# Kernel tuning notes

Measured on AMD Instinct MI355X. Metric: run time of the kernel, lower is better.

## Reference

```python
import jax, jax.numpy as jnp
import numpy as np

HID_DIM = 1024
B, S = 8, 2048
SCALE = float(np.sqrt(HID_DIM))
NEG = -1e10


def setup_inputs() -> dict:
    key = jax.random.key(0)
    ks = jax.random.split(key, 13)
    d = HID_DIM
    std = 1.0 / np.sqrt(d)
    return {
        "query": jax.random.normal(ks[0], (B, S, d), jnp.float32),
        "key_": jax.random.normal(ks[1], (B, S, d), jnp.float32),
        "value": jax.random.normal(ks[2], (B, S, d), jnp.float32),
        "mask": jax.random.randint(ks[3], (B, S), 0, 2, jnp.int32),
        "Wq": jax.random.uniform(ks[4], (d, d), jnp.float32, -std, std),
        "bq": jax.random.uniform(ks[5], (d,), jnp.float32, -std, std),
        "Wk": jax.random.uniform(ks[6], (d, d), jnp.float32, -std, std),
        "bk": jax.random.uniform(ks[7], (d,), jnp.float32, -std, std),
        "Wv": jax.random.uniform(ks[8], (d, d), jnp.float32, -std, std),
        "bv": jax.random.uniform(ks[9], (d,), jnp.float32, -std, std),
        "Wfc": jax.random.uniform(ks[10], (d, d), jnp.float32, -std, std),
        "bfc": jax.random.uniform(ks[11], (d,), jnp.float32, -std, std),
    }


def reference(query, key_, value, mask, Wq, bq, Wk, bk, Wv, bv, Wfc, bfc):
    # Linear projections (torch Linear: x @ W.T + b)
    Q = jnp.einsum("bsd,ed->bse", query, Wq) + bq
    K = jnp.einsum("bsd,ed->bse", key_, Wk) + bk
    V = jnp.einsum("bsd,ed->bse", value, Wv) + bv
    # Scaled dot-product energy: [B, S, S]
    energy = jnp.einsum("bqd,bkd->bqk", Q, K) / SCALE
    # Faithful to source: mask broadcast over last dim masks QUERY rows
    energy = jnp.where(mask[:, :, None] == 0, NEG, energy)
    attention = jax.nn.softmax(energy, axis=-1)  # dropout=0 (eval)
    x = jnp.einsum("bqk,bkd->bqd", attention, V)
    out = jnp.einsum("bsd,ed->bse", x, Wfc) + bfc
    return out
```

## Files before the change

kernel.cpp:

```cpp
#include <hip/hip_runtime.h>
#include <hip/hip_bf16.h>


#define DEVINL __device__ __forceinline__

typedef __bf16 bf16x8 __attribute__((ext_vector_type(8)));
typedef float f32x4 __attribute__((ext_vector_type(4)));

static constexpr int Bb = 8;
static constexpr int S = 2048;
static constexpr int D = 1024;

DEVINL unsigned short f32_to_bf16(float f) {
  unsigned u = __float_as_uint(f);
  u = (u + 0x7FFFu + ((u >> 16) & 1u)) >> 16;
  return (unsigned short)u;
}
DEVINL float bflo(unsigned u) { return __uint_as_float(u << 16); }
DEVINL float bfhi(unsigned u) { return __uint_as_float(u & 0xFFFF0000u); }

DEVINL void gload16(const unsigned short* g, char* l) {
  __builtin_amdgcn_global_load_lds((__attribute__((address_space(1))) void*)g,
                                   (__attribute__((address_space(3))) void*)l,
                                   16, 0, 0);
}
DEVINL void gload16u(const unsigned short* g, unsigned short* l) {
  gload16(g, (char*)l);
}

#define BAR() __builtin_amdgcn_s_barrier()
#define LGK0() asm volatile("s_waitcnt lgkmcnt(0)" ::: "memory")

#define PH_OPEN() \
  BAR();          \
  LGK0();         \
  __builtin_amdgcn_s_setprio(1)
#define PH_CLOSE()               \
  __builtin_amdgcn_s_setprio(0); \
  BAR()

#define MFMA_QUAD(A_, B_, MO, NO)                                              \
  {                                                                            \
    _Pragma("unroll") for (int mi_ = 0; mi_ < 4; mi_++) {                      \
      _Pragma("unroll") for (int nj_ = 0; nj_ < 2; nj_++) {                    \
        acc[(MO) + mi_][(NO) + nj_] = __builtin_amdgcn_mfma_f32_16x16x32_bf16( \
            A_[mi_][0], B_[nj_][0], acc[(MO) + mi_][(NO) + nj_], 0, 0, 0);     \
        acc[(MO) + mi_][(NO) + nj_] = __builtin_amdgcn_mfma_f32_16x16x32_bf16( \
            A_[mi_][1], B_[nj_][1], acc[(MO) + mi_][(NO) + nj_], 0, 0, 0);     \
      }                                                                        \
    }                                                                          \
  }

__global__ __launch_bounds__(256) void conv_f32_bf16(const float* __restrict__ in,
                                                     unsigned short* __restrict__ out,
                                                     int n8) {
  int i = blockIdx.x * 256 + threadIdx.x;
  int stride = gridDim.x * 256;
  for (; i < n8; i += stride) {
    const float4* p = (const float4*)in + (size_t)i * 2;
    float4 a = p[0], b = p[1];
    uint4 o;
    o.x = (unsigned)f32_to_bf16(a.x) | ((unsigned)f32_to_bf16(a.y) << 16);
    o.y = (unsigned)f32_to_bf16(a.z) | ((unsigned)f32_to_bf16(a.w) << 16);
    o.z = (unsigned)f32_to_bf16(b.x) | ((unsigned)f32_to_bf16(b.y) << 16);
    o.w = (unsigned)f32_to_bf16(b.z) | ((unsigned)f32_to_bf16(b.w) << 16);
    ((uint4*)out)[i] = o;
  }
}

__global__ __launch_bounds__(256) void tconv(const float* __restrict__ in,
                                             unsigned short* __restrict__ out,
                                             int R, int C) {
  __shared__ unsigned short t[64][72];
  const int c0 = blockIdx.x * 64, r0 = blockIdx.y * 64, b = blockIdx.z;
  in += (size_t)b * R * C;
  out += (size_t)b * R * C;
  const int tr = threadIdx.x >> 4;
  const int tc = threadIdx.x & 15;
#pragma unroll
  for (int i = 0; i < 4; i++) {
    int row = tr + i * 16;
    float4 v = *(const float4*)(in + (size_t)(r0 + row) * C + c0 + tc * 4);
    t[tc * 4 + 0][row] = f32_to_bf16(v.x);
    t[tc * 4 + 1][row] = f32_to_bf16(v.y);
    t[tc * 4 + 2][row] = f32_to_bf16(v.z);
    t[tc * 4 + 3][row] = f32_to_bf16(v.w);
  }
  __syncthreads();
  const int c = threadIdx.x >> 2, rs = (threadIdx.x & 3) * 16;
  unsigned short tmp[16];
#pragma unroll
  for (int j = 0; j < 16; j++) tmp[j] = t[c][rs + j];
  *(uint4*)(out + (size_t)(c0 + c) * R + r0 + rs) = *(const uint4*)&tmp[0];
  *(uint4*)(out + (size_t)(c0 + c) * R + r0 + rs + 8) = *(const uint4*)&tmp[8];
}

__global__ __launch_bounds__(256) void cvec_kernel(const float* __restrict__ Wfc,
                                                   const float* __restrict__ bv,
                                                   const float* __restrict__ bfc,
                                                   float* __restrict__ cv) {
  const int f = blockIdx.x;
  const float* row = Wfc + (size_t)f * 1024;
  float s = 0.f;
  for (int e = threadIdx.x; e < 1024; e += 256) s += row[e] * bv[e];
#pragma unroll
  for (int off = 32; off >= 1; off >>= 1) s += __shfl_xor(s, off);
  __shared__ float red[4];
  const int wave = threadIdx.x >> 6, lane = threadIdx.x & 63;
  if (lane == 0) red[wave] = s;
  __syncthreads();
  if (threadIdx.x == 0) cv[f] = red[0] + red[1] + red[2] + red[3] + bfc[f];
}

__global__ __launch_bounds__(256) void gvec_kernel(const unsigned short* __restrict__ WkT,
                                                   const float* __restrict__ bq,
                                                   float* __restrict__ g32) {
  const int e = blockIdx.x;
  const unsigned short* row = WkT + (size_t)e * 1024;
  const int j0 = threadIdx.x * 4;
  uint2 v = *(const uint2*)(row + j0);
  float4 b4 = *(const float4*)(bq + j0);
  float s = bflo(v.x) * b4.x + bfhi(v.x) * b4.y + bflo(v.y) * b4.z + bfhi(v.y) * b4.w;
#pragma unroll
  for (int off = 32; off >= 1; off >>= 1) s += __shfl_xor(s, off);
  __shared__ float red[4];
  const int wave = threadIdx.x >> 6, lane = threadIdx.x & 63;
  if (lane == 0) red[wave] = s;
  __syncthreads();
  if (threadIdx.x == 0) g32[e] = (red[0] + red[1] + red[2] + red[3]) * (1.0f / 32.0f);
}

__global__ __launch_bounds__(256) void wvec_kernel(const unsigned short* __restrict__ xk,
                                                   const float* __restrict__ g32,
                                                   float* __restrict__ w32) {
  const int row = blockIdx.x * 4 + (threadIdx.x >> 6);
  const int lane = threadIdx.x & 63;
  const unsigned short* r = xk + (size_t)row * 1024;
  float s = 0.f;
#pragma unroll
  for (int c = 0; c < 2; c++) {
    const int e0 = c * 512 + lane * 8;
    uint4 v = *(const uint4*)(r + e0);
    unsigned u[4] = {v.x, v.y, v.z, v.w};
#pragma unroll
    for (int i = 0; i < 4; i++) {
      float2 gg = *(const float2*)(g32 + e0 + i * 2);
      s += bflo(u[i]) * gg.x + bfhi(u[i]) * gg.y;
    }
  }
#pragma unroll
  for (int off = 32; off >= 1; off >>= 1) s += __shfl_xor(s, off);
  if (lane == 0) w32[row] = s;
}

__global__ __launch_bounds__(256) void mask_scan(const int* __restrict__ msk,
                                                 int* __restrict__ qidx,
                                                 int* __restrict__ midx,
                                                 int* __restrict__ cnts) {
  __shared__ int offs[257];
  const int b = blockIdx.x;
  const int* mrow = msk + b * 2048;
  const int base = threadIdx.x * 8;
  int m[8], c = 0;
#pragma unroll
  for (int i = 0; i < 8; i++) {
    m[i] = mrow[base + i];
    c += m[i];
  }
  offs[threadIdx.x + 1] = c;
  __syncthreads();
  if (threadIdx.x == 0) {
    offs[0] = 0;
    for (int j = 1; j <= 256; j++) offs[j] += offs[j - 1];
    int tot = offs[256];
    cnts[b] = tot;
    cnts[8 + b] = (tot + 127) & ~127;
    cnts[16 + b] = (tot + 255) & ~255;
    cnts[24 + b] = 2048 - tot;
  }
  __syncthreads();
  int u = offs[threadIdx.x];
#pragma unroll
  for (int i = 0; i < 8; i++) {
    int idx = base + i;
    if (m[i])
      qidx[b * 2048 + (u++)] = idx;
    else
      midx[b * 2048 + (idx - u)] = idx;
  }
}

__global__ __launch_bounds__(128) void compact_q(const float* __restrict__ q,
                                                 const int* __restrict__ qidx,
                                                 const int* __restrict__ cnts,
                                                 unsigned short* __restrict__ xqC) {
  const int r = blockIdx.x;
  const int b = r >> 11, i = r & 2047;
  if (i >= cnts[16 + b]) return;
  unsigned short* dst = xqC + ((size_t)b * 2048 + i) * 1024;
  if (i < cnts[b]) {
    const float* src = q + ((size_t)b * 2048 + qidx[b * 2048 + i]) * 1024 + threadIdx.x * 8;
    float4 a = *(const float4*)src;
    float4 c = *(const float4*)(src + 4);
    uint4 o;
    o.x = (unsigned)f32_to_bf16(a.x) | ((unsigned)f32_to_bf16(a.y) << 16);
    o.y = (unsigned)f32_to_bf16(a.z) | ((unsigned)f32_to_bf16(a.w) << 16);
    o.z = (unsigned)f32_to_bf16(c.x) | ((unsigned)f32_to_bf16(c.y) << 16);
    o.w = (unsigned)f32_to_bf16(c.z) | ((unsigned)f32_to_bf16(c.w) << 16);
    ((uint4*)dst)[threadIdx.x] = o;
  } else {
    ((uint4*)dst)[threadIdx.x] = make_uint4(0, 0, 0, 0);
  }
}

__global__ __launch_bounds__(64) void colmean_kernel(const unsigned short* __restrict__ vpT,
                                                     const float* __restrict__ cv,
                                                     float* __restrict__ cm) {
  const int f = blockIdx.x, b = blockIdx.y;
  const unsigned short* base = vpT + (size_t)f * 16384 + b * 2048 + threadIdx.x * 32;
  float s = 0.f;
#pragma unroll
  for (int c = 0; c < 4; c++) {
    uint4 v = ((const uint4*)base)[c];
    unsigned u[4] = {v.x, v.y, v.z, v.w};
#pragma unroll
    for (int i = 0; i < 4; i++) s += bflo(u[i]) + bfhi(u[i]);
  }
#pragma unroll
  for (int off = 32; off >= 1; off >>= 1) s += __shfl_xor(s, off);
  if (threadIdx.x == 0) cm[b * 1024 + f] = s * (1.0f / 2048.0f) + cv[f];
}

__global__ __launch_bounds__(128) void fill_masked(const int* __restrict__ midx,
                                                   const int* __restrict__ cnts,
                                                   const float* __restrict__ cm,
                                                   float* __restrict__ out) {
  const int r = blockIdx.x;
  const int b = r >> 11, j = r & 2047;
  if (j >= cnts[24 + b]) return;
  const int qr = midx[b * 2048 + j];
  float* dst = out + ((size_t)b * 2048 + qr) * 1024 + threadIdx.x * 8;
  const float* src = cm + b * 1024 + threadIdx.x * 8;
  *(float4*)dst = *(const float4*)src;
  *(float4*)(dst + 4) = *(const float4*)(src + 4);
}

__global__ __launch_bounds__(256) void rowinv_kernel(const float* __restrict__ partialT,
                                                     float* __restrict__ rowinv) {
  const int r = blockIdx.x * 256 + threadIdx.x;
  float s = 0.f;
#pragma unroll
  for (int c = 0; c < 32; c++) s += partialT[(size_t)c * 16384 + r];
  rowinv[r] = 1.0f / s;
}

__global__ __launch_bounds__(256) void gemm128(const unsigned short* __restrict__ A,
                                               const unsigned short* __restrict__ Bt,
                                               unsigned short* __restrict__ C,
                                               int M, int N, int K,
                                               long long bsA, long long bsB, long long bsC) {
  const int tid = threadIdx.x;
  const int wave = tid >> 6;
  const int lane = tid & 63;
  const int wr = wave >> 1, wc = wave & 1;
  const int m0 = blockIdx.y * 128, n0 = blockIdx.x * 128;
  A += (size_t)blockIdx.z * bsA;
  Bt += (size_t)blockIdx.z * bsB;
  C += (size_t)blockIdx.z * bsC;

  __shared__ unsigned short lds[2][2][128 * 32];

  const int srow = wave * 16 + (lane >> 2);
  const int scol = (lane & 3) * 8;
  const unsigned short* gA = A + (size_t)(m0 + srow) * K + scol;
  const unsigned short* gB = Bt + (size_t)(n0 + srow) * K + scol;

  f32x4 acc[4][4];
#pragma unroll
  for (int i = 0; i < 4; i++)
#pragma unroll
    for (int j = 0; j < 4; j++) acc[i][j] = (f32x4){0.f, 0.f, 0.f, 0.f};

  const int nk = K >> 5;
  auto stage = [&](int buf, int kt) {
    const unsigned short* a0 = gA + (size_t)kt * 32;
    const unsigned short* b0 = gB + (size_t)kt * 32;
    unsigned short* la = &lds[buf][0][wave * 512];
    unsigned short* lb = &lds[buf][1][wave * 512];
    gload16u(a0, la);
    gload16u(a0 + (size_t)64 * K, la + 2048);
    gload16u(b0, lb);
    gload16u(b0 + (size_t)64 * K, lb + 2048);
  };

  stage(0, 0);
  asm volatile("s_waitcnt vmcnt(0)" ::: "memory");
  __syncthreads();

  const int fm = lane & 15;
  const int fk = (lane >> 4) * 8;

  int cur = 0;
  for (int t = 0; t < nk; ++t) {
    if (t + 1 < nk) stage(cur ^ 1, t + 1);
    bf16x8 af[4], bfr[4];
#pragma unroll
    for (int i = 0; i < 4; i++)
      af[i] = *(const bf16x8*)&lds[cur][0][(wr * 64 + i * 16 + fm) * 32 + fk];
#pragma unroll
    for (int j = 0; j < 4; j++)
      bfr[j] = *(const bf16x8*)&lds[cur][1][(wc * 64 + j * 16 + fm) * 32 + fk];
#pragma unroll
    for (int i = 0; i < 4; i++)
#pragma unroll
      for (int j = 0; j < 4; j++)
        acc[i][j] = __builtin_amdgcn_mfma_f32_16x16x32_bf16(af[i], bfr[j], acc[i][j], 0, 0, 0);
    asm volatile("s_waitcnt vmcnt(0)" ::: "memory");
    __syncthreads();
    cur ^= 1;
  }

  const int en = n0 + wc * 64 + fm;
  const int em = m0 + wr * 64 + ((lane >> 4) << 2);
#pragma unroll
  for (int j = 0; j < 4; j++)
#pragma unroll
    for (int i = 0; i < 4; i++)
#pragma unroll
      for (int r = 0; r < 4; r++)
        C[(size_t)(em + i * 16 + r) * N + en + j * 16] = f32_to_bf16(acc[i][j][r]);
}

__global__ __launch_bounds__(512, 1) void gemmE(
    const unsigned short* __restrict__ A, const unsigned short* __restrict__ Bt,
    const float* __restrict__ w32, const int* __restrict__ cnts,
    float* __restrict__ partialT, unsigned short* __restrict__ E, float scale) {
  extern __shared__ char smem[];
  const int tid = threadIdx.x;
  const int wave = tid >> 6, lane = tid & 63;
  const int wrM = wave >> 1, wcN = wave & 1;

  const int nwg = 16 * 8 * 8;
  const int wg = blockIdx.x + 16 * (blockIdx.y + 8 * blockIdx.z);
  const int swz = (wg & 7) * (nwg >> 3) + (wg >> 3);
  const int bx = swz % 16;
  const int rem = swz / 16;
  const int by = rem % 8;
  const int bz = rem / 8;

  const int n0 = bx * 128;
  if (n0 >= cnts[8 + bz]) return;
  const int m0 = by * 256;
  A += (size_t)bz * 2048 * 1024;
  Bt += (size_t)bz * 2048 * 1024;

  const int rl = lane >> 3;
  const int gl = (lane & 7) ^ rl;
  const unsigned short* gA = A + (size_t)(m0 + wave * 8 + rl) * 1024 + gl * 8;
  const unsigned short* gB = Bt + (size_t)(n0 + wave * 8 + rl) * 1024 + gl * 8;

  auto stage = [&](int db, int t) {
    char* base = smem + db * 49152;
    const unsigned short* ga = gA + (size_t)t * 64;
    const unsigned short* gb = gB + (size_t)t * 64;
#pragma unroll
    for (int c = 0; c < 4; c++)
      gload16(ga + (size_t)c * 64 * 1024, base + c * 8192 + wave * 1024);
#pragma unroll
    for (int c = 0; c < 2; c++)
      gload16(gb + (size_t)c * 64 * 1024, base + 32768 + c * 8192 + wave * 1024);
  };

  const int fr = lane & 15;
  const int fg = lane >> 4;
  auto readA = [&](int db, int mi, int kc) -> bf16x8 {
    const int row = wrM * 64 + mi * 16 + fr;
    const int g = (kc * 4 + fg) ^ (row & 7);
    return *(const bf16x8*)(smem + db * 49152 + row * 128 + g * 16);
  };
  auto readB = [&](int db, int nj, int kc) -> bf16x8 {
    const int row = wcN * 64 + nj * 16 + fr;
    const int g = (kc * 4 + fg) ^ (row & 7);
    return *(const bf16x8*)(smem + db * 49152 + 32768 + row * 128 + g * 16);
  };

  f32x4 acc[4][4];
#pragma unroll
  for (int i = 0; i < 4; i++)
#pragma unroll
    for (int j = 0; j < 4; j++) acc[i][j] = (f32x4){0.f, 0.f, 0.f, 0.f};

  const int nt = 16;
  stage(0, 0);
  stage(1, 1);
  asm volatile("s_waitcnt vmcnt(6)" ::: "memory");
  BAR();

  for (int t = 0; t < nt; ++t) {
    const int db = t % 3;
    bf16x8 a[4][2], b0[2][2], b1[2][2];
#pragma unroll
    for (int mi = 0; mi < 4; mi++) { a[mi][0] = readA(db, mi, 0); a[mi][1] = readA(db, mi, 1); }
#pragma unroll
    for (int nj = 0; nj < 2; nj++) { b0[nj][0] = readB(db, nj, 0); b0[nj][1] = readB(db, nj, 1); }
    BAR();
    LGK0();
    if (t + 2 < nt) stage((t + 2) % 3, t + 2);
    __builtin_amdgcn_s_setprio(1);
    MFMA_QUAD(a, b0, 0, 0);
    __builtin_amdgcn_s_setprio(0);
    BAR();
#pragma unroll
    for (int nj = 0; nj < 2; nj++) { b1[nj][0] = readB(db, nj + 2, 0); b1[nj][1] = readB(db, nj + 2, 1); }
    BAR();
    LGK0();
    __builtin_amdgcn_s_setprio(1);
    MFMA_QUAD(a, b1, 0, 2);
    __builtin_amdgcn_s_setprio(0);
    if (t + 2 < nt)
      asm volatile("s_waitcnt vmcnt(6)" ::: "memory");
    else
      asm volatile("s_waitcnt vmcnt(0)" ::: "memory");
    BAR();
  }

  const int keyrow0 = m0 + wrM * 64 + fg * 4;
  const int colq = wcN * 64 + fr;
  float psum[4] = {0.f, 0.f, 0.f, 0.f};
#pragma unroll
  for (int mi = 0; mi < 4; mi++) {
    const int krow = keyrow0 + mi * 16;
    const float4 w4 = *(const float4*)&w32[bz * 2048 + krow];
    const int lrow = wrM * 64 + fg * 4 + mi * 16;
#pragma unroll
    for (int nj = 0; nj < 4; nj++) {
      float p0 = __expf(fmaf(acc[mi][nj][0], scale, w4.x));
      float p1 = __expf(fmaf(acc[mi][nj][1], scale, w4.y));
      float p2 = __expf(fmaf(acc[mi][nj][2], scale, w4.z));
      float p3 = __expf(fmaf(acc[mi][nj][3], scale, w4.w));
      psum[nj] += (p0 + p1) + (p2 + p3);
      unsigned lo = (unsigned)f32_to_bf16(p0) | ((unsigned)f32_to_bf16(p1) << 16);
      unsigned hi = (unsigned)f32_to_bf16(p2) | ((unsigned)f32_to_bf16(p3) << 16);
      const int c = colq + nj * 16;
      const int byte = c * 512 + ((((lrow >> 3) ^ (c & 7)) << 4) | ((lrow & 4) << 1));
      *(uint2*)(smem + byte) = make_uint2(lo, hi);
    }
  }
#pragma unroll
  for (int nj = 0; nj < 4; nj++) {
    psum[nj] += __shfl_xor(psum[nj], 16);
    psum[nj] += __shfl_xor(psum[nj], 32);
  }
  if (fg == 0) {
#pragma unroll
    for (int nj = 0; nj < 4; nj++)
      partialT[(size_t)(by * 4 + wrM) * 16384 + bz * 2048 + n0 + colq + nj * 16] = psum[nj];
  }
  __syncthreads();
  unsigned short* Eb = E + (size_t)bz * S * S;
  const int qh = wave * 2 + (lane >> 5);
  const int kl = (lane & 31) * 8;
#pragma unroll
  for (int p = 0; p < 8; p++) {
    const int ql = qh + p * 16;
    const int byte = ql * 512 + ((((kl >> 3) ^ (ql & 7)) << 4));
    uint4 vv = *(const uint4*)(smem + byte);
    *(uint4*)(Eb + (size_t)(n0 + ql) * 2048 + m0 + kl) = vv;
  }
}

template <int OUTMODE, bool HAS_BIAS, int EXITMODE>
__global__ __launch_bounds__(512, 2) void gemm256(
    const unsigned short* __restrict__ A, const unsigned short* __restrict__ Bt,
    const float* __restrict__ bias, const int* __restrict__ cnts,
    const int* __restrict__ qidx, float* __restrict__ partial,
    void* __restrict__ Cv, int M, int N, int K, int lda, int ldb,
    long long bsA, long long bsB, long long bsC, float scale) {
  extern __shared__ char smem[];
  const int tid = threadIdx.x;
  const int wave = tid >> 6, lane = tid & 63;
  const int wr = wave >> 2, wc = wave & 3;

  const int gx = gridDim.x, gy = gridDim.y;
  const int nwg = gx * gy * (int)gridDim.z;
  const int wg = blockIdx.x + gx * (blockIdx.y + gy * blockIdx.z);
  const int swz = (wg & 7) * (nwg >> 3) + (wg >> 3);
  const int bx = swz % gx;
  const int rem = swz / gx;
  const int by = rem % gy;
  const int bz = rem / gy;

  const int m0 = by * 256, n0 = bx * 256;
  if (EXITMODE == 1) {
    if ((n0 & 2047) >= cnts[16 + (n0 >> 11)]) return;
  } else if (EXITMODE == 2) {
    if (m0 >= cnts[16 + bz]) return;
  }
  A += (size_t)bz * bsA;
  Bt += (size_t)bz * bsB;

  const int rl = lane >> 3;
  const int gl = (lane & 7) ^ rl;
  const unsigned short* gA = A + (size_t)(m0 + wave * 8 + rl) * lda + gl * 8;
  const unsigned short* gB = Bt + (size_t)(n0 + wave * 8 + rl) * ldb + gl * 8;

  auto stageA = [&](int db, int t, int h) {
    const unsigned short* g = gA + (size_t)(h * 128) * lda + (size_t)t * 64;
    char* l = smem + db * 65536 + h * 16384 + wave * 1024;
    gload16(g, l);
    gload16(g + (size_t)64 * lda, l + 8192);
  };
  auto stageB = [&](int db, int t, int h) {
    const unsigned short* g = gB + (size_t)(h * 128) * ldb + (size_t)t * 64;
    char* l = smem + db * 65536 + 32768 + h * 16384 + wave * 1024;
    gload16(g, l);
    gload16(g + (size_t)64 * ldb, l + 8192);
  };

  const int fr = lane & 15;
  const int fg = lane >> 4;
  auto readA = [&](int db, int mi, int kc) -> bf16x8 {
    const int row = wr * 128 + mi * 16 + fr;
    const int g = (kc * 4 + fg) ^ (row & 7);
    return *(const bf16x8*)(smem + db * 65536 + row * 128 + g * 16);
  };
  auto readB = [&](int db, int nj, int kc) -> bf16x8 {
    const int row = wc * 64 + nj * 16 + fr;
    const int g = (kc * 4 + fg) ^ (row & 7);
    return *(const bf16x8*)(smem + db * 65536 + 32768 + row * 128 + g * 16);
  };

  f32x4 acc[8][4];
#pragma unroll
  for (int i = 0; i < 8; i++)
#pragma unroll
    for (int j = 0; j < 4; j++) acc[i][j] = (f32x4){0.f, 0.f, 0.f, 0.f};

  stageA(0, 0, 0);
  stageA(0, 0, 1);
  stageB(0, 0, 0);
  stageB(0, 0, 1);
  stageB(1, 1, 0);
  stageB(1, 1, 1);
  asm volatile("s_waitcnt vmcnt(4)" ::: "memory");
  BAR();

  const int nt = K >> 6;
  const int niter = nt >> 1;

  for (int j = 0; j < niter; ++j) {
    const int t0 = 2 * j, t1 = 2 * j + 1;
    const bool more = (j + 1 < niter);
    bf16x8 a[4][2], b0[2][2], b1[2][2];

#pragma unroll
    for (int mi = 0; mi < 4; mi++) { a[mi][0] = readA(0, mi, 0); a[mi][1] = readA(0, mi, 1); }
#pragma unroll
    for (int nj = 0; nj < 2; nj++) { b0[nj][0] = readB(0, nj, 0); b0[nj][1] = readB(0, nj, 1); }
    stageA(1, t1, 0);
    asm volatile("s_waitcnt lgkmcnt(8)" ::: "memory");
    PH_OPEN();
    MFMA_QUAD(a, b0, 0, 0);
    PH_CLOSE();

#pragma unroll
    for (int nj = 0; nj < 2; nj++) { b1[nj][0] = readB(0, nj + 2, 0); b1[nj][1] = readB(0, nj + 2, 1); }
    stageA(1, t1, 1);
    PH_OPEN();
    MFMA_QUAD(a, b1, 0, 2);
    PH_CLOSE();

#pragma unroll
    for (int mi = 0; mi < 4; mi++) { a[mi][0] = readA(0, mi + 4, 0); a[mi][1] = readA(0, mi + 4, 1); }
    if (more) stageB(0, t0 + 2, 0);
    PH_OPEN();
    MFMA_QUAD(a, b0, 4, 0);
    PH_CLOSE();

    if (more) stageB(0, t0 + 2, 1);
    BAR();
    __builtin_amdgcn_s_setprio(1);
    MFMA_QUAD(a, b1, 4, 2);
    __builtin_amdgcn_s_setprio(0);
    if (more)
      asm volatile("s_waitcnt vmcnt(4)" ::: "memory");
    else
      asm volatile("s_waitcnt vmcnt(0)" ::: "memory");
    BAR();

#pragma unroll
    for (int mi = 0; mi < 4; mi++) { a[mi][0] = readA(1, mi, 0); a[mi][1] = readA(1, mi, 1); }
#pragma unroll
    for (int nj = 0; nj < 2; nj++) { b0[nj][0] = readB(1, nj, 0); b0[nj][1] = readB(1, nj, 1); }
    if (more) stageA(0, t0 + 2, 0);
    asm volatile("s_waitcnt lgkmcnt(8)" ::: "memory");
    PH_OPEN();
    MFMA_QUAD(a, b0, 0, 0);
    PH_CLOSE();

#pragma unroll
    for (int nj = 0; nj < 2; nj++) { b1[nj][0] = readB(1, nj + 2, 0); b1[nj][1] = readB(1, nj + 2, 1); }
    if (more) stageA(0, t0 + 2, 1);
    PH_OPEN();
    MFMA_QUAD(a, b1, 0, 2);
    PH_CLOSE();

#pragma unroll
    for (int mi = 0; mi < 4; mi++) { a[mi][0] = readA(1, mi + 4, 0); a[mi][1] = readA(1, mi + 4, 1); }
    if (more) stageB(1, t1 + 2, 0);
    PH_OPEN();
    MFMA_QUAD(a, b0, 4, 0);
    PH_CLOSE();

    if (more) stageB(1, t1 + 2, 1);
    BAR();
    __builtin_amdgcn_s_setprio(1);
    MFMA_QUAD(a, b1, 4, 2);
    __builtin_amdgcn_s_setprio(0);
    asm volatile("s_waitcnt vmcnt(4)" ::: "memory");
    BAR();
  }

  const int row0base = m0 + wr * 128 + fg * 4;
  const int colbase = n0 + wc * 64 + fr;

  if (OUTMODE == 6) {
    float* C = (float*)Cv + (size_t)bz * bsC;
    const int* qx = qidx + bz * 2048;
    const int cb = cnts[bz];
#pragma unroll
    for (int mi = 0; mi < 8; mi++) {
      const int j0 = row0base + mi * 16;
      const float4 ri = *(const float4*)&partial[bz * 2048 + j0];
      int qr[4];
      bool ok[4];
#pragma unroll
      for (int r = 0; r < 4; r++) {
        ok[r] = (j0 + r) < cb;
        qr[r] = ok[r] ? qx[j0 + r] : 0;
      }
#pragma unroll
      for (int nj = 0; nj < 4; nj++) {
        const int col = colbase + nj * 16;
        const float cvv = HAS_BIAS ? bias[col] : 0.0f;
        if (ok[0]) C[(size_t)qr[0] * N + col] = fmaf(acc[mi][nj][0], ri.x, cvv);
        if (ok[1]) C[(size_t)qr[1] * N + col] = fmaf(acc[mi][nj][1], ri.y, cvv);
        if (ok[2]) C[(size_t)qr[2] * N + col] = fmaf(acc[mi][nj][2], ri.z, cvv);
        if (ok[3]) C[(size_t)qr[3] * N + col] = fmaf(acc[mi][nj][3], ri.w, cvv);
      }
    }
  } else {
    const int lcol = wc * 64 + fr;
    const int lrow0 = wr * 128 + fg * 4;
#pragma unroll
    for (int mi = 0; mi < 8; mi++) {
      const int lrow = lrow0 + mi * 16;
      float4 bw = make_float4(0.f, 0.f, 0.f, 0.f);
      if (HAS_BIAS) bw = *(const float4*)&bias[row0base + mi * 16];
#pragma unroll
      for (int nj = 0; nj < 4; nj++) {
        float v0 = acc[mi][nj][0] + bw.x;
        float v1 = acc[mi][nj][1] + bw.y;
        float v2 = acc[mi][nj][2] + bw.z;
        float v3 = acc[mi][nj][3] + bw.w;
        unsigned lo = (unsigned)f32_to_bf16(v0) | ((unsigned)f32_to_bf16(v1) << 16);
        unsigned hi = (unsigned)f32_to_bf16(v2) | ((unsigned)f32_to_bf16(v3) << 16);
        const int c = lcol + nj * 16;
        const int byte = c * 512 + ((((lrow >> 3) ^ (c & 7)) << 4) | ((lrow & 4) << 1));
        *(uint2*)(smem + byte) = make_uint2(lo, hi);
      }
    }
    __syncthreads();
    unsigned short* C = (unsigned short*)Cv + (size_t)bz * bsC;
    const int qh = wave * 2 + (lane >> 5);
    const int kl = (lane & 31) * 8;
#pragma unroll
    for (int p = 0; p < 16; p++) {
      const int ql = qh + p * 16;
      const int byte = ql * 512 + ((((kl >> 3) ^ (ql & 7)) << 4));
      uint4 vv = *(const uint4*)(smem + byte);
      *(uint4*)(C + (size_t)(n0 + ql) * M + m0 + kl) = vv;
    }
  }
}

extern "C" void kernel_launch(void* const* d_in, const int* in_sizes, int n_in,
                              void* d_out, int out_size, void* d_ws, size_t ws_size,
                              hipStream_t stream) {
  const float* q = (const float*)d_in[0];
  const float* k_ = (const float*)d_in[1];
  const float* v = (const float*)d_in[2];
  const int* msk = (const int*)d_in[3];
  const float* Wq = (const float*)d_in[4];
  const float* bq = (const float*)d_in[5];
  const float* Wk = (const float*)d_in[6];
  const float* Wv = (const float*)d_in[8];
  const float* bv = (const float*)d_in[9];
  const float* Wfc = (const float*)d_in[10];
  const float* bfc = (const float*)d_in[11];

  char* ws = (char*)d_ws;
  const size_t MB = 1u << 20;
  const size_t KB = 1u << 10;
  unsigned short* WkT = (unsigned short*)(ws + 0 * MB);
  unsigned short* WfcB = (unsigned short*)(ws + 2 * MB);
  unsigned short* WqT = (unsigned short*)(ws + 4 * MB);
  unsigned short* WvT = (unsigned short*)(ws + 6 * MB);
  unsigned short* Mt = (unsigned short*)(ws + 8 * MB);
  unsigned short* W2 = (unsigned short*)(ws + 10 * MB);
  float* partialT = (float*)(ws + 12 * MB);
  float* rowinv = (float*)(ws + 14 * MB);
  float* cv = (float*)(ws + 14 * MB + 64 * KB);
  float* g32 = (float*)(ws + 14 * MB + 128 * KB);
  float* w32 = (float*)(ws + 14 * MB + 192 * KB);
  int* qidx = (int*)(ws + 14 * MB + 256 * KB);
  int* midx = (int*)(ws + 14 * MB + 320 * KB);
  int* cnts = (int*)(ws + 14 * MB + 384 * KB);
  float* cm = (float*)(ws + 14 * MB + 512 * KB);
  unsigned short* Qc = (unsigned short*)(ws + 16 * MB);
  unsigned short* xkB = (unsigned short*)(ws + 48 * MB);
  unsigned short* vpT = (unsigned short*)(ws + 80 * MB);
  unsigned short* xqC = (unsigned short*)(ws + 112 * MB);
  unsigned short* vB = (unsigned short*)(ws + 144 * MB);
  unsigned short* E = (unsigned short*)(ws + 112 * MB);

  const int NBS = Bb * S * D;

  auto conv = [&](const float* in, unsigned short* out, int n) {
    int n8 = n / 8;
    int blocks = (n8 + 255) / 256;
    if (blocks > 2048) blocks = 2048;
    conv_f32_bf16<<<dim3(blocks), dim3(256), 0, stream>>>(in, out, n8);
  };

  tconv<<<dim3(16, 16, 1), dim3(256), 0, stream>>>(Wq, WqT, D, D);
  tconv<<<dim3(16, 16, 1), dim3(256), 0, stream>>>(Wk, WkT, D, D);
  conv(Wfc, WfcB, D * D);
  tconv<<<dim3(16, 16, 1), dim3(256), 0, stream>>>(Wv, WvT, D, D);
  gemm128<<<dim3(8, 8, 2), dim3(256), 0, stream>>>(
      WkT, WqT, Mt, D, D, D, (long long)D * D, (long long)D * D, (long long)D * D);
  cvec_kernel<<<dim3(1024), dim3(256), 0, stream>>>(Wfc, bv, bfc, cv);
  gvec_kernel<<<dim3(1024), dim3(256), 0, stream>>>(WkT, bq, g32);

  mask_scan<<<dim3(8), dim3(256), 0, stream>>>(msk, qidx, midx, cnts);
  compact_q<<<dim3(16384), dim3(128), 0, stream>>>(q, qidx, cnts, xqC);

  const float invscale = 1.0f / 32.0f;

  gemm256<1, false, 1><<<dim3(64, 4, 1), dim3(512), 131072, stream>>>(
      Mt, xqC, nullptr, cnts, nullptr, nullptr, Qc, D, Bb * S, D, D, D,
      0, 0, 0, 1.0f);
  conv(k_, xkB, NBS);
  wvec_kernel<<<dim3(4096), dim3(256), 0, stream>>>(xkB, g32, w32);
  conv(v, vB, NBS);
  gemm256<1, false, 0><<<dim3(4, 64, 1), dim3(512), 131072, stream>>>(
      vB, W2, nullptr, nullptr, nullptr, nullptr, vpT, Bb * S, D, D, D, D,
      0, 0, 0, 1.0f);
  colmean_kernel<<<dim3(1024, 8), dim3(64), 0, stream>>>(vpT, cv, cm);
  gemmE<<<dim3(16, 8, 8), dim3(512), 147456, stream>>>(
      xkB, Qc, w32, cnts, partialT, E, invscale);
  rowinv_kernel<<<dim3(64), dim3(256), 0, stream>>>(partialT, rowinv);
  gemm256<6, true, 2><<<dim3(4, 8, 8), dim3(512), 131072, stream>>>(
      E, vpT, cv, cnts, qidx, rowinv, d_out, S, D, S, S, Bb * S,
      (long long)S * S, (long long)S, (long long)S * D, 1.0f);
  fill_masked<<<dim3(16384), dim3(128), 0, stream>>>(midx, cnts, cm, (float*)d_out);
}
```

Measured before the change: 319.4 us.

## Replace energy and output GEMMs with a shared 128x128-tile kernel

Adds a templated 128x128-tile GEMM (256 threads, two blocks per CU, double-buffered LDS) and uses it for both the energy/exp GEMM and the attention-times-V output GEMM. It replaces the 256x128 three-stage gemmE and the 256x256 gemm256 OUTMODE 6 path. Smaller tiles give finer-grained early exit on masked query counts, plus more blocks and higher occupancy. In exchange it uses a simpler pipeline that waits on all loads every iteration and gets less operand reuse per tile.

```diff
diff --git a/kernel.cpp b/kernel.cpp
--- a/kernel.cpp
+++ b/kernel.cpp
@@ -331,57 +331,66 @@
         C[(size_t)(em + i * 16 + r) * N + en + j * 16] = f32_to_bf16(acc[i][j][r]);
 }
 
-__global__ __launch_bounds__(512, 1) void gemmE(
+template <int OUTMODE>
+__global__ __launch_bounds__(256, 2) void gemm128c(
     const unsigned short* __restrict__ A, const unsigned short* __restrict__ Bt,
-    const float* __restrict__ w32, const int* __restrict__ cnts,
-    float* __restrict__ partialT, unsigned short* __restrict__ E, float scale) {
+    const float* __restrict__ aux,
+    const float* __restrict__ bias,
+    const int* __restrict__ cnts, const int* __restrict__ qidx,
+    float* __restrict__ partialT, void* __restrict__ Cv,
+    int N, int K, int lda, int ldb,
+    long long bsA, long long bsB, long long bsC, float scale) {
   extern __shared__ char smem[];
   const int tid = threadIdx.x;
   const int wave = tid >> 6, lane = tid & 63;
-  const int wrM = wave >> 1, wcN = wave & 1;
-
-  const int nwg = 16 * 8 * 8;
-  const int wg = blockIdx.x + 16 * (blockIdx.y + 8 * blockIdx.z);
+  const int wm = wave >> 1, wn = wave & 1;
+
+  const int gx = gridDim.x, gy = gridDim.y;
+  const int nwg = gx * gy * (int)gridDim.z;
+  const int wg = blockIdx.x + gx * (blockIdx.y + gy * blockIdx.z);
   const int swz = (wg & 7) * (nwg >> 3) + (wg >> 3);
-  const int bx = swz % 16;
-  const int rem = swz / 16;
-  const int by = rem % 8;
-  const int bz = rem / 8;
-
-  const int n0 = bx * 128;
-  if (n0 >= cnts[8 + bz]) return;
-  const int m0 = by * 256;
-  A += (size_t)bz * 2048 * 1024;
-  Bt += (size_t)bz * 2048 * 1024;
+  const int bx = swz % gx;
+  const int rem = swz / gx;
+  const int by = rem % gy;
+  const int bz = rem / gy;
+
+  const int m0 = by * 128, n0 = bx * 128;
+  if (OUTMODE == 3) {
+    if (n0 >= cnts[8 + bz]) return;
+  } else {
+    if (m0 >= cnts[8 + bz]) return;
+  }
+  A += (size_t)bz * bsA;
+  Bt += (size_t)bz * bsB;
 
   const int rl = lane >> 3;
   const int gl = (lane & 7) ^ rl;
-  const unsigned short* gA = A + (size_t)(m0 + wave * 8 + rl) * 1024 + gl * 8;
-  const unsigned short* gB = Bt + (size_t)(n0 + wave * 8 + rl) * 1024 + gl * 8;
+  const unsigned short* gA = A + (size_t)(m0 + wave * 8 + rl) * lda + gl * 8;
+  const unsigned short* gB = Bt + (size_t)(n0 + wave * 8 + rl) * ldb + gl * 8;
 
   auto stage = [&](int db, int t) {
-    char* base = smem + db * 49152;
-    const unsigned short* ga = gA + (size_t)t * 64;
-    const unsigned short* gb = gB + (size_t)t * 64;
-#pragma unroll
-    for (int c = 0; c < 4; c++)
-      gload16(ga + (size_t)c * 64 * 1024, base + c * 8192 + wave * 1024);
-#pragma unroll
-    for (int c = 0; c < 2; c++)
-      gload16(gb + (size_t)c * 64 * 1024, base + 32768 + c * 8192 + wave * 1024);
+    char* la = smem + db * 32768;
+    char* lb = la + 16384;
+    const unsigned short* a0 = gA + (size_t)t * 64;
+    const unsigned short* b0 = gB + (size_t)t * 64;
+#pragma unroll
+    for (int i = 0; i < 4; i++) {
+      gload16(a0 + (size_t)(i * 32) * lda, la + i * 4096 + wave * 1024);
+      gload16(b0 + (size_t)(i * 32) * ldb, lb + i * 4096 + wave * 1024);
+    }
   };
 
   const int fr = lane & 15;
   const int fg = lane >> 4;
   auto readA = [&](int db, int mi, int kc) -> bf16x8 {
-    const int row = wrM * 64 + mi * 16 + fr;
+    const int row = wm * 64 + mi * 16 + fr;
     const int g = (kc * 4 + fg) ^ (row & 7);
-    return *(const bf16x8*)(smem + db * 49152 + row * 128 + g * 16);
+    return *(const bf16x8*)(smem + db * 32768 + row * 128 + g * 16);
   };
   auto readB = [&](int db, int nj, int kc) -> bf16x8 {
-    const int row = wcN * 64 + nj * 16 + fr;
+    const int row = wn * 64 + nj * 16 + fr;
     const int g = (kc * 4 + fg) ^ (row & 7);
-    return *(const bf16x8*)(smem + db * 49152 + 32768 + row * 128 + g * 16);
+    return *(const bf16x8*)(smem + db * 32768 + 16384 + row * 128 + g * 16);
   };
 
   f32x4 acc[4][4];
@@ -390,82 +399,108 @@
 #pragma unroll
     for (int j = 0; j < 4; j++) acc[i][j] = (f32x4){0.f, 0.f, 0.f, 0.f};
 
-  const int nt = 16;
   stage(0, 0);
-  stage(1, 1);
-  asm volatile("s_waitcnt vmcnt(6)" ::: "memory");
+  asm volatile("s_waitcnt vmcnt(0)" ::: "memory");
   BAR();
 
+  const int nt = K >> 6;
   for (int t = 0; t < nt; ++t) {
-    const int db = t % 3;
-    bf16x8 a[4][2], b0[2][2], b1[2][2];
-#pragma unroll
-    for (int mi = 0; mi < 4; mi++) { a[mi][0] = readA(db, mi, 0); a[mi][1] = readA(db, mi, 1); }
-#pragma unroll
-    for (int nj = 0; nj < 2; nj++) { b0[nj][0] = readB(db, nj, 0); b0[nj][1] = readB(db, nj, 1); }
+    const int cur = t & 1;
+    if (t + 1 < nt) stage(cur ^ 1, t + 1);
+    bf16x8 a[4][2], b[4][2];
+#pragma unroll
+    for (int mi = 0; mi < 4; mi++) {
+      a[mi][0] = readA(cur, mi, 0);
+      a[mi][1] = readA(cur, mi, 1);
+    }
+#pragma unroll
+    for (int nj = 0; nj < 4; nj++) {
+      b[nj][0] = readB(cur, nj, 0);
+      b[nj][1] = readB(cur, nj, 1);
+    }
+    __builtin_amdgcn_s_setprio(1);
+#pragma unroll
+    for (int mi = 0; mi < 4; mi++)
+#pragma unroll
+      for (int nj = 0; nj < 4; nj++) {
+        acc[mi][nj] = __builtin_amdgcn_mfma_f32_16x16x32_bf16(a[mi][0], b[nj][0], acc[mi][nj], 0, 0, 0);
+        acc[mi][nj] = __builtin_amdgcn_mfma_f32_16x16x32_bf16(a[mi][1], b[nj][1], acc[mi][nj], 0, 0, 0);
+      }
+    __builtin_amdgcn_s_setprio(0);
+    asm volatile("s_waitcnt vmcnt(0)" ::: "memory");
     BAR();
-    LGK0();
-    if (t + 2 < nt) stage((t + 2) % 3, t + 2);
-    __builtin_amdgcn_s_setprio(1);
-    MFMA_QUAD(a, b0, 0, 0);
-    __builtin_amdgcn_s_setprio(0);
-    BAR();
-#pragma unroll
-    for (int nj = 0; nj < 2; nj++) { b1[nj][0] = readB(db, nj + 2, 0); b1[nj][1] = readB(db, nj + 2, 1); }
-    BAR();
-    LGK0();
-    __builtin_amdgcn_s_setprio(1);
-    MFMA_QUAD(a, b1, 0, 2);
-    __builtin_amdgcn_s_setprio(0);
-    if (t + 2 < nt)
-      asm volatile("s_waitcnt vmcnt(6)" ::: "memory");
-    else
-      asm volatile("s_waitcnt vmcnt(0)" ::: "memory");
-    BAR();
-  }
-
-  const int keyrow0 = m0 + wrM * 64 + fg * 4;
-  const int colq = wcN * 64 + fr;
-  float psum[4] = {0.f, 0.f, 0.f, 0.f};
-#pragma unroll
-  for (int mi = 0; mi < 4; mi++) {
-    const int krow = keyrow0 + mi * 16;
-    const float4 w4 = *(const float4*)&w32[bz * 2048 + krow];
-    const int lrow = wrM * 64 + fg * 4 + mi * 16;
+  }
+
+  if (OUTMODE == 3) {
+    const int keyrow0 = m0 + wm * 64 + fg * 4;
+    const int colq = wn * 64 + fr;
+    float psum[4] = {0.f, 0.f, 0.f, 0.f};
+#pragma unroll
+    for (int mi = 0; mi < 4; mi++) {
+      const float4 w4 = *(const float4*)&aux[bz * 2048 + keyrow0 + mi * 16];
+      const int lrow = wm * 64 + fg * 4 + mi * 16;
+#pragma unroll
+      for (int nj = 0; nj < 4; nj++) {
+        float p0 = __expf(fmaf(acc[mi][nj][0], scale, w4.x));
+        float p1 = __expf(fmaf(acc[mi][nj][1], scale, w4.y));
+        float p2 = __expf(fmaf(acc[mi][nj][2], scale, w4.z));
+        float p3 = __expf(fmaf(acc[mi][nj][3], scale, w4.w));
+        psum[nj] += (p0 + p1) + (p2 + p3);
+        unsigned lo = (unsigned)f32_to_bf16(p0) | ((unsigned)f32_to_bf16(p1) << 16);
+        unsigned hi = (unsigned)f32_to_bf16(p2) | ((unsigned)f32_to_bf16(p3) << 16);
+        const int c = colq + nj * 16;
+        const int byte = c * 256 + ((((lrow >> 3) ^ (c & 7)) << 4) | ((lrow & 4) << 1));
+        *(uint2*)(smem + byte) = make_uint2(lo, hi);
+      }
+    }
 #pragma unroll
     for (int nj = 0; nj < 4; nj++) {
-      float p0 = __expf(fmaf(acc[mi][nj][0], scale, w4.x));
-      float p1 = __expf(fmaf(acc[mi][nj][1], scale, w4.y));
-      float p2 = __expf(fmaf(acc[mi][nj][2], scale, w4.z));
-      float p3 = __expf(fmaf(acc[mi][nj][3], scale, w4.w));
-      psum[nj] += (p0 + p1) + (p2 + p3);
-      unsigned lo = (unsigned)f32_to_bf16(p0) | ((unsigned)f32_to_bf16(p1) << 16);
-      unsigned hi = (unsigned)f32_to_bf16(p2) | ((unsigned)f32_to_bf16(p3) << 16);
-      const int c = colq + nj * 16;
-      const int byte = c * 512 + ((((lrow >> 3) ^ (c & 7)) << 4) | ((lrow & 4) << 1));
-      *(uint2*)(smem + byte) = make_uint2(lo, hi);
-    }
-  }
-#pragma unroll
-  for (int nj = 0; nj < 4; nj++) {
-    psum[nj] += __shfl_xor(psum[nj], 16);
-    psum[nj] += __shfl_xor(psum[nj], 32);
-  }
-  if (fg == 0) {
-#pragma unroll
-    for (int nj = 0; nj < 4; nj++)
-      partialT[(size_t)(by * 4 + wrM) * 16384 + bz * 2048 + n0 + colq + nj * 16] = psum[nj];
-  }
-  __syncthreads();
-  unsigned short* Eb = E + (size_t)bz * S * S;
-  const int qh = wave * 2 + (lane >> 5);
-  const int kl = (lane & 31) * 8;
-#pragma unroll
-  for (int p = 0; p < 8; p++) {
-    const int ql = qh + p * 16;
-    const int byte = ql * 512 + ((((kl >> 3) ^ (ql & 7)) << 4));
-    uint4 vv = *(const uint4*)(smem + byte);
-    *(uint4*)(Eb + (size_t)(n0 + ql) * 2048 + m0 + kl) = vv;
+      psum[nj] += __shfl_xor(psum[nj], 16);
+      psum[nj] += __shfl_xor(psum[nj], 32);
+    }
+    if (fg == 0) {
+#pragma unroll
+      for (int nj = 0; nj < 4; nj++)
+        partialT[(size_t)(by * 2 + wm) * 16384 + bz * 2048 + n0 + colq + nj * 16] = psum[nj];
+    }
+    __syncthreads();
+    unsigned short* Eb = (unsigned short*)Cv + (size_t)bz * bsC;
+    const int qh = wave * 2 + (lane >> 5);
+    const int kq = (lane & 31) * 4;
+#pragma unroll
+    for (int p = 0; p < 16; p++) {
+      const int ql = qh + p * 8;
+      const int byte = ql * 256 + ((((kq >> 3) ^ (ql & 7)) << 4) | ((kq & 4) << 1));
+      uint2 vv = *(const uint2*)(smem + byte);
+      *(uint2*)(Eb + (size_t)(n0 + ql) * 2048 + m0 + kq) = vv;
+    }
+  } else {
+    float* C = (float*)Cv + (size_t)bz * bsC;
+    const int* qx = qidx + bz * 2048;
+    const int cb = cnts[bz];
+    const int row0base = m0 + wm * 64 + fg * 4;
+    const int colbase = n0 + wn * 64 + fr;
+#pragma unroll
+    for (int mi = 0; mi < 4; mi++) {
+      const int j0 = row0base + mi * 16;
+      const float4 ri = *(const float4*)&aux[bz * 2048 + j0];
+      int qr[4];
+      bool ok[4];
+#pragma unroll
+      for (int r = 0; r < 4; r++) {
+        ok[r] = (j0 + r) < cb;
+        qr[r] = ok[r] ? qx[j0 + r] : 0;
+      }
+#pragma unroll
+      for (int nj = 0; nj < 4; nj++) {
+        const int col = colbase + nj * 16;
+        const float cvv = bias[col];
+        if (ok[0]) C[(size_t)qr[0] * N + col] = fmaf(acc[mi][nj][0], ri.x, cvv);
+        if (ok[1]) C[(size_t)qr[1] * N + col] = fmaf(acc[mi][nj][1], ri.y, cvv);
+        if (ok[2]) C[(size_t)qr[2] * N + col] = fmaf(acc[mi][nj][2], ri.z, cvv);
+        if (ok[3]) C[(size_t)qr[3] * N + col] = fmaf(acc[mi][nj][3], ri.w, cvv);
+      }
+    }
   }
 }
 
@@ -493,8 +528,6 @@
   const int m0 = by * 256, n0 = bx * 256;
   if (EXITMODE == 1) {
     if ((n0 & 2047) >= cnts[16 + (n0 >> 11)]) return;
-  } else if (EXITMODE == 2) {
-    if (m0 >= cnts[16 + bz]) return;
   }
   A += (size_t)bz * bsA;
   Bt += (size_t)bz * bsB;
@@ -622,34 +655,8 @@
   }
 
   const int row0base = m0 + wr * 128 + fg * 4;
-  const int colbase = n0 + wc * 64 + fr;
-
-  if (OUTMODE == 6) {
-    float* C = (float*)Cv + (size_t)bz * bsC;
-    const int* qx = qidx + bz * 2048;
-    const int cb = cnts[bz];
-#pragma unroll
-    for (int mi = 0; mi < 8; mi++) {
-      const int j0 = row0base + mi * 16;
-      const float4 ri = *(const float4*)&partial[bz * 2048 + j0];
-      int qr[4];
-      bool ok[4];
-#pragma unroll
-      for (int r = 0; r < 4; r++) {
-        ok[r] = (j0 + r) < cb;
-        qr[r] = ok[r] ? qx[j0 + r] : 0;
-      }
-#pragma unroll
-      for (int nj = 0; nj < 4; nj++) {
-        const int col = colbase + nj * 16;
-        const float cvv = HAS_BIAS ? bias[col] : 0.0f;
-        if (ok[0]) C[(size_t)qr[0] * N + col] = fmaf(acc[mi][nj][0], ri.x, cvv);
-        if (ok[1]) C[(size_t)qr[1] * N + col] = fmaf(acc[mi][nj][1], ri.y, cvv);
-        if (ok[2]) C[(size_t)qr[2] * N + col] = fmaf(acc[mi][nj][2], ri.z, cvv);
-        if (ok[3]) C[(size_t)qr[3] * N + col] = fmaf(acc[mi][nj][3], ri.w, cvv);
-      }
-    }
-  } else {
+
+  {
     const int lcol = wc * 64 + fr;
     const int lrow0 = wr * 128 + fg * 4;
 #pragma unroll
@@ -757,11 +764,14 @@
       vB, W2, nullptr, nullptr, nullptr, nullptr, vpT, Bb * S, D, D, D, D,
       0, 0, 0, 1.0f);
   colmean_kernel<<<dim3(1024, 8), dim3(64), 0, stream>>>(vpT, cv, cm);
-  gemmE<<<dim3(16, 8, 8), dim3(512), 147456, stream>>>(
-      xkB, Qc, w32, cnts, partialT, E, invscale);
+  gemm128c<3><<<dim3(16, 16, 8), dim3(256), 65536, stream>>>(
+      xkB, Qc, w32, nullptr, cnts, nullptr, partialT, E,
+      D, 1024, 1024, 1024, (long long)S * D, (long long)S * D,
+      (long long)S * S, invscale);
   rowinv_kernel<<<dim3(64), dim3(256), 0, stream>>>(partialT, rowinv);
-  gemm256<6, true, 2><<<dim3(4, 8, 8), dim3(512), 131072, stream>>>(
-      E, vpT, cv, cnts, qidx, rowinv, d_out, S, D, S, S, Bb * S,
-      (long long)S * S, (long long)S, (long long)S * D, 1.0f);
+  gemm128c<6><<<dim3(8, 16, 8), dim3(256), 65536, stream>>>(
+      E, vpT, rowinv, cv, cnts, qidx, nullptr, d_out,
+      D, 2048, 2048, Bb * S, (long long)S * S, (long long)S,
+      (long long)S * D, 1.0f);
   fill_masked<<<dim3(16384), dim3(128), 0, stream>>>(midx, cnts, cm, (float*)d_out);
 }
```

Measured after the change: 306.9 us. 3.9% less time.
